# Kernel optimization log

Measured on AMD Instinct MI355X. Metric: run time of the kernel, lower is better.

Reference implementation:

```python
import jax, jax.numpy as jnp
import numpy as np


def setup_inputs() -> dict:
    key = jax.random.key(0)
    k1, k2 = jax.random.split(key)
    x = jax.random.normal(k1, (16384, 1024), dtype=jnp.float32)
    # 10 butterfly stages, each with 512 independent 2x2 mixing matrices
    Ws = jax.random.normal(k2, (10, 512, 2, 2), dtype=jnp.float32)
    return {"x": x, "Ws": Ws}


def reference(x, Ws):
    """PairLinear_MixerBlock forward for input_dim == output_dim == 2^L.
    selector and reducer are Identity; only the butterfly mixing stages remain.
    """
    bs, dim = x.shape
    n_stages = Ws.shape[0]  # log2(dim)
    y = x
    for i in range(n_stages):
        stride = 2 ** i
        # y.view(-1, 2, 2**i).permute(0, 2, 1).contiguous().view(bs, -1)
        y = y.reshape(-1, 2, stride).transpose(0, 2, 1).reshape(bs, -1)
        # PairLinear: view(bs, -1, 2) then per-pair 2x2 matmul with Ws[i]
        y = jnp.einsum('bpk,pkj->bpj', y.reshape(bs, -1, 2), Ws[i]).reshape(bs, -1)
        # y.view(-1, 2**i, 2).permute(0, 2, 1).contiguous()
        y = y.reshape(-1, stride, 2).transpose(0, 2, 1).reshape(bs, dim)
    return y
```

## Files before the change

kernel.cpp:

```cpp
#include <hip/hip_runtime.h>

#define DIM 1024
#define RPW 4
#define WAVES 4
#define ROWS_PER_BLOCK (RPW * WAVES)

__global__ __launch_bounds__(256) void butterfly_kernel(
    const float* __restrict__ x,
    const float* __restrict__ Ws,
    float* __restrict__ out,
    int rows)
{
    const int lane = threadIdx.x & 63;
    const int wave = threadIdx.x >> 6;
    const int row0 = (blockIdx.x * WAVES + wave) * RPW;

    const float4* __restrict__ Wm = (const float4*)Ws;

    float d[RPW][16];

    #pragma unroll
    for (int r = 0; r < RPW; ++r) {
        int row = row0 + r;
        if (row < rows) {
            const float4* src = (const float4*)(x + (size_t)row * DIM);
            #pragma unroll
            for (int q = 0; q < 4; ++q) {
                float4 v = src[q * 64 + lane];
                d[r][q*4+0] = v.x; d[r][q*4+1] = v.y;
                d[r][q*4+2] = v.z; d[r][q*4+3] = v.w;
            }
        } else {
            #pragma unroll
            for (int e = 0; e < 16; ++e) d[r][e] = 0.f;
        }
    }

    #pragma unroll
    for (int q = 0; q < 4; ++q) {
        int base = 0*512 + q*128 + lane*2;
        float4 m0 = Wm[base], m1 = Wm[base+1];
        #pragma unroll
        for (int r = 0; r < RPW; ++r) {
            int e = q*4;
            float u = d[r][e+0], v = d[r][e+1];
            d[r][e+0] = u*m0.x + v*m0.z;
            d[r][e+1] = u*m0.y + v*m0.w;
            u = d[r][e+2]; v = d[r][e+3];
            d[r][e+2] = u*m1.x + v*m1.z;
            d[r][e+3] = u*m1.y + v*m1.w;
        }
    }

    #pragma unroll
    for (int q = 0; q < 4; ++q) {
        int base = 1*512 + q*128 + lane*2;
        float4 m0 = Wm[base], m1 = Wm[base+1];
        #pragma unroll
        for (int r = 0; r < RPW; ++r) {
            int e = q*4;
            float u = d[r][e+0], v = d[r][e+2];
            d[r][e+0] = u*m0.x + v*m0.z;
            d[r][e+2] = u*m0.y + v*m0.w;
            u = d[r][e+1]; v = d[r][e+3];
            d[r][e+1] = u*m1.x + v*m1.z;
            d[r][e+3] = u*m1.y + v*m1.w;
        }
    }

    #pragma unroll
    for (int i = 2; i < 8; ++i) {
        const int m = 1 << (i - 2);
        const int a = (lane >> (i - 2)) & 1;
        #pragma unroll
        for (int q = 0; q < 4; ++q) {
            int P0 = (((q*64 + lane) >> (i-1)) << i) | ((lane & (m-1)) << 2);
            int base = i*512 + P0;
            float4 M0 = Wm[base+0], M1 = Wm[base+1], M2 = Wm[base+2], M3 = Wm[base+3];
            float wA0 = a ? M0.w : M0.x, wB0 = a ? M0.y : M0.z;
            float wA1 = a ? M1.w : M1.x, wB1 = a ? M1.y : M1.z;
            float wA2 = a ? M2.w : M2.x, wB2 = a ? M2.y : M2.z;
            float wA3 = a ? M3.w : M3.x, wB3 = a ? M3.y : M3.z;
            #pragma unroll
            for (int r = 0; r < RPW; ++r) {
                int e = q*4;
                float o0 = __shfl_xor(d[r][e+0], m);
                float o1 = __shfl_xor(d[r][e+1], m);
                float o2 = __shfl_xor(d[r][e+2], m);
                float o3 = __shfl_xor(d[r][e+3], m);
                d[r][e+0] = d[r][e+0]*wA0 + o0*wB0;
                d[r][e+1] = d[r][e+1]*wA1 + o1*wB1;
                d[r][e+2] = d[r][e+2]*wA2 + o2*wB2;
                d[r][e+3] = d[r][e+3]*wA3 + o3*wB3;
            }
        }
    }

    #pragma unroll
    for (int qp = 0; qp < 2; ++qp) {
        int base = 8*512 + qp*256 + lane*4;
        float4 M0 = Wm[base+0], M1 = Wm[base+1], M2 = Wm[base+2], M3 = Wm[base+3];
        #pragma unroll
        for (int r = 0; r < RPW; ++r) {
            int eu = (2*qp)*4, ev = (2*qp+1)*4;
            float u, v;
            u = d[r][eu+0]; v = d[r][ev+0]; d[r][eu+0] = u*M0.x + v*M0.z; d[r][ev+0] = u*M0.y + v*M0.w;
            u = d[r][eu+1]; v = d[r][ev+1]; d[r][eu+1] = u*M1.x + v*M1.z; d[r][ev+1] = u*M1.y + v*M1.w;
            u = d[r][eu+2]; v = d[r][ev+2]; d[r][eu+2] = u*M2.x + v*M2.z; d[r][ev+2] = u*M2.y + v*M2.w;
            u = d[r][eu+3]; v = d[r][ev+3]; d[r][eu+3] = u*M3.x + v*M3.z; d[r][ev+3] = u*M3.y + v*M3.w;
        }
    }

    #pragma unroll
    for (int qp = 0; qp < 2; ++qp) {
        int base = 9*512 + qp*256 + lane*4;
        float4 M0 = Wm[base+0], M1 = Wm[base+1], M2 = Wm[base+2], M3 = Wm[base+3];
        #pragma unroll
        for (int r = 0; r < RPW; ++r) {
            int eu = qp*4, ev = (qp+2)*4;
            float u, v;
            u = d[r][eu+0]; v = d[r][ev+0]; d[r][eu+0] = u*M0.x + v*M0.z; d[r][ev+0] = u*M0.y + v*M0.w;
            u = d[r][eu+1]; v = d[r][ev+1]; d[r][eu+1] = u*M1.x + v*M1.z; d[r][ev+1] = u*M1.y + v*M1.w;
            u = d[r][eu+2]; v = d[r][ev+2]; d[r][eu+2] = u*M2.x + v*M2.z; d[r][ev+2] = u*M2.y + v*M2.w;
            u = d[r][eu+3]; v = d[r][ev+3]; d[r][eu+3] = u*M3.x + v*M3.z; d[r][ev+3] = u*M3.y + v*M3.w;
        }
    }

    #pragma unroll
    for (int r = 0; r < RPW; ++r) {
        int row = row0 + r;
        if (row < rows) {
            float4* dst = (float4*)(out + (size_t)row * DIM);
            #pragma unroll
            for (int q = 0; q < 4; ++q) {
                float4 v;
                v.x = d[r][q*4+0]; v.y = d[r][q*4+1];
                v.z = d[r][q*4+2]; v.w = d[r][q*4+3];
                dst[q * 64 + lane] = v;
            }
        }
    }
}

extern "C" void kernel_launch(void* const* d_in, const int* in_sizes, int n_in,
                              void* d_out, int out_size, void* d_ws, size_t ws_size,
                              hipStream_t stream) {
    const float* x  = (const float*)d_in[0];
    const float* Ws = (const float*)d_in[1];
    float* out = (float*)d_out;

    int rows = in_sizes[0] / DIM;
    int grid = (rows + ROWS_PER_BLOCK - 1) / ROWS_PER_BLOCK;
    butterfly_kernel<<<grid, 256, 0, stream>>>(x, Ws, out, rows);
}
```

Before: 51.27 us.

## Pre-pack per-lane shuffle-stage weights in workspace and raise occupancy hint

```diff
diff --git a/kernel.cpp b/kernel.cpp
--- a/kernel.cpp
+++ b/kernel.cpp
@@ -4,10 +4,38 @@
 #define RPW 4
 #define WAVES 4
 #define ROWS_PER_BLOCK (RPW * WAVES)
+#define PACKED_BYTES (6 * 4 * 64 * 8 * 4)
 
-__global__ __launch_bounds__(256) void butterfly_kernel(
+
+__global__ void pack_weights(const float* __restrict__ Ws, float* __restrict__ pw) {
+    int t = blockIdx.x * blockDim.x + threadIdx.x;
+    if (t >= 6 * 4 * 64) return;
+    int lane = t & 63;
+    int q = (t >> 6) & 3;
+    int i = (t >> 8) + 2;
+    int m = 1 << (i - 2);
+    int a = (lane >> (i - 2)) & 1;
+    int P0 = (((q * 64 + lane) >> (i - 1)) << i) | ((lane & (m - 1)) << 2);
+    const float4* Wm = (const float4*)Ws;
+    float4 wa, wb;
+    float* pa = (float*)&wa;
+    float* pb = (float*)&wb;
+    #pragma unroll
+    for (int e = 0; e < 4; ++e) {
+        float4 M = Wm[i * 512 + P0 + e];
+        pa[e] = a ? M.w : M.x;
+        pb[e] = a ? M.y : M.z;
+    }
+    float4* o = (float4*)pw + (size_t)t * 2;
+    o[0] = wa;
+    o[1] = wb;
+}
+
+template <bool PACKED, int MINB>
+__global__ __launch_bounds__(256, MINB) void butterfly_kernel(
     const float* __restrict__ x,
     const float* __restrict__ Ws,
+    const float* __restrict__ pw,
     float* __restrict__ out,
     int rows)
 {
@@ -71,16 +99,25 @@
     #pragma unroll
     for (int i = 2; i < 8; ++i) {
         const int m = 1 << (i - 2);
-        const int a = (lane >> (i - 2)) & 1;
         #pragma unroll
         for (int q = 0; q < 4; ++q) {
-            int P0 = (((q*64 + lane) >> (i-1)) << i) | ((lane & (m-1)) << 2);
-            int base = i*512 + P0;
-            float4 M0 = Wm[base+0], M1 = Wm[base+1], M2 = Wm[base+2], M3 = Wm[base+3];
-            float wA0 = a ? M0.w : M0.x, wB0 = a ? M0.y : M0.z;
-            float wA1 = a ? M1.w : M1.x, wB1 = a ? M1.y : M1.z;
-            float wA2 = a ? M2.w : M2.x, wB2 = a ? M2.y : M2.z;
-            float wA3 = a ? M3.w : M3.x, wB3 = a ? M3.y : M3.z;
+            float wA0, wA1, wA2, wA3, wB0, wB1, wB2, wB3;
+            if (PACKED) {
+                const float4* wp = (const float4*)pw
+                    + ((size_t)(((i - 2) * 4 + q) * 64 + lane)) * 2;
+                float4 wa = wp[0], wb = wp[1];
+                wA0 = wa.x; wA1 = wa.y; wA2 = wa.z; wA3 = wa.w;
+                wB0 = wb.x; wB1 = wb.y; wB2 = wb.z; wB3 = wb.w;
+            } else {
+                const int a = (lane >> (i - 2)) & 1;
+                int P0 = (((q*64 + lane) >> (i-1)) << i) | ((lane & (m-1)) << 2);
+                int base = i*512 + P0;
+                float4 M0 = Wm[base+0], M1 = Wm[base+1], M2 = Wm[base+2], M3 = Wm[base+3];
+                wA0 = a ? M0.w : M0.x; wB0 = a ? M0.y : M0.z;
+                wA1 = a ? M1.w : M1.x; wB1 = a ? M1.y : M1.z;
+                wA2 = a ? M2.w : M2.x; wB2 = a ? M2.y : M2.z;
+                wA3 = a ? M3.w : M3.x; wB3 = a ? M3.y : M3.z;
+            }
             #pragma unroll
             for (int r = 0; r < RPW; ++r) {
                 int e = q*4;
@@ -151,5 +188,12 @@
 
     int rows = in_sizes[0] / DIM;
     int grid = (rows + ROWS_PER_BLOCK - 1) / ROWS_PER_BLOCK;
-    butterfly_kernel<<<grid, 256, 0, stream>>>(x, Ws, out, rows);
+
+    if (ws_size >= (size_t)PACKED_BYTES) {
+        float* pw = (float*)d_ws;
+        pack_weights<<<6, 256, 0, stream>>>(Ws, pw);
+        butterfly_kernel<true, 5><<<grid, 256, 0, stream>>>(x, Ws, pw, out, rows);
+    } else {
+        butterfly_kernel<false, 4><<<grid, 256, 0, stream>>>(x, Ws, nullptr, out, rows);
+    }
 }
```

After: 147.4 us. 188% more time.

## Compose butterfly stages into block-diagonal matrices and apply via bf16 MFMA

Applied to the files above, without the earlier changes.

```diff
diff --git a/kernel.cpp b/kernel.cpp
--- a/kernel.cpp
+++ b/kernel.cpp
@@ -1,80 +1,190 @@
 #include <hip/hip_runtime.h>
 
 #define DIM 1024
-#define RPW 4
-#define WAVES 4
-#define ROWS_PER_BLOCK (RPW * WAVES)
-
-__global__ __launch_bounds__(256) void butterfly_kernel(
+#define ROWS_PER_TILE 16
+
+typedef float  f32x4  __attribute__((ext_vector_type(4)));
+typedef short  bf16x8 __attribute__((ext_vector_type(8)));
+typedef unsigned int u32x2 __attribute__((ext_vector_type(2)));
+
+#define WF_BYTES (2 * 32 * 2 * 64 * 16)
+
+
+__device__ __forceinline__ short f2bfs(float f) {
+    union { __bf16 b; short s; } c; c.b = (__bf16)f; return c.s;
+}
+__device__ __forceinline__ unsigned f2bfbits(float f) {
+    union { __bf16 b; unsigned short u; } c; c.b = (__bf16)f; return (unsigned)c.u;
+}
+
+__global__ __launch_bounds__(64) void compose_pack(const float* __restrict__ Ws,
+                                                   short* __restrict__ wf) {
+    __shared__ float M[32 * 32];
+    const int b = blockIdx.x;
+    const int tid = threadIdx.x;
+    const bool isB = b >= 32;
+    const int grp = isB ? b - 32 : b;
+
+    for (int s = tid; s < 1024; s += 64) M[s] = ((s >> 5) == (s & 31)) ? 1.f : 0.f;
+    __syncthreads();
+
+    for (int il = 0; il < 5; ++il) {
+        #pragma unroll
+        for (int s = 0; s < 8; ++s) {
+            int task = tid + s * 64;
+            int pl = task >> 5;
+            int r  = task & 31;
+            int lo = ((pl >> il) << (il + 1)) | (pl & ((1 << il) - 1));
+            int hi = lo + (1 << il);
+            int wi = isB ? ((5 + il) * 512 + pl * 32 + grp)
+                         : (il * 512 + grp * 16 + pl);
+            const float* W = Ws + (size_t)wi * 4;
+            float w00 = W[0], w01 = W[1], w10 = W[2], w11 = W[3];
+            float u = M[r * 32 + lo], v = M[r * 32 + hi];
+            M[r * 32 + lo] = u * w00 + v * w10;
+            M[r * 32 + hi] = u * w01 + v * w11;
+        }
+        __syncthreads();
+    }
+
+    const int q = tid >> 4, lr = tid & 15;
+    #pragma unroll
+    for (int nh = 0; nh < 2; ++nh) {
+        bf16x8 fr;
+        #pragma unroll
+        for (int e = 0; e < 8; ++e)
+            fr[e] = f2bfs(M[(q * 8 + e) * 32 + nh * 16 + lr]);
+        size_t idx = (size_t)(isB ? 4096 : 0) + ((size_t)grp * 2 + nh) * 64 + tid;
+        ((bf16x8*)wf)[idx] = fr;
+    }
+}
+
+__global__ __launch_bounds__(256) void bfly_mfma(
     const float* __restrict__ x,
-    const float* __restrict__ Ws,
-    float* __restrict__ out,
-    int rows)
+    const short* __restrict__ wf1,
+    const short* __restrict__ wf2,
+    float* __restrict__ out)
+{
+    __shared__ char zt[32 * 1024];
+    const int tid = threadIdx.x;
+    const int w = tid >> 6;
+    const int l = tid & 63;
+    const int q = l >> 4, lr = l & 15;
+    const int row0 = blockIdx.x * ROWS_PER_TILE;
+
+    const f32x4 zacc = {0.f, 0.f, 0.f, 0.f};
+
+    const float* xrow = x + (size_t)(row0 + lr) * DIM;
+    #pragma unroll
+    for (int gi = 0; gi < 8; ++gi) {
+        const int g = w * 8 + gi;
+        const f32x4* xp = (const f32x4*)(xrow + g * 32 + q * 8);
+        f32x4 xa = __builtin_nontemporal_load(xp);
+        f32x4 xb = __builtin_nontemporal_load(xp + 1);
+        bf16x8 af;
+        af[0] = f2bfs(xa[0]); af[1] = f2bfs(xa[1]);
+        af[2] = f2bfs(xa[2]); af[3] = f2bfs(xa[3]);
+        af[4] = f2bfs(xb[0]); af[5] = f2bfs(xb[1]);
+        af[6] = f2bfs(xb[2]); af[7] = f2bfs(xb[3]);
+        bf16x8 b0 = ((const bf16x8*)wf1)[(g * 2 + 0) * 64 + l];
+        bf16x8 b1 = ((const bf16x8*)wf1)[(g * 2 + 1) * 64 + l];
+        f32x4 c0 = __builtin_amdgcn_mfma_f32_16x16x32_bf16(af, b0, zacc, 0, 0, 0);
+        f32x4 c1 = __builtin_amdgcn_mfma_f32_16x16x32_bf16(af, b1, zacc, 0, 0, 0);
+        #pragma unroll
+        for (int nh = 0; nh < 2; ++nh) {
+            f32x4 cc = nh ? c1 : c0;
+            int c = nh * 16 + lr;
+            unsigned lo = f2bfbits(cc[0]) | (f2bfbits(cc[1]) << 16);
+            unsigned hi = f2bfbits(cc[2]) | (f2bfbits(cc[3]) << 16);
+            int byteoff = (c * 1024 + g * 32 + q * 8) ^ ((c & 15) << 3);
+            u32x2 pk = {lo, hi};
+            *(u32x2*)(zt + byteoff) = pk;
+        }
+    }
+    __syncthreads();
+
+    f32x4 o[2][8];
+    #pragma unroll
+    for (int hh = 0; hh < 8; ++hh) {
+        const int h = w * 8 + hh;
+        bf16x8 a2;
+        #pragma unroll
+        for (int e = 0; e < 8; ++e) {
+            int byteoff = (h * 1024 + (q * 8 + e) * 32 + lr * 2) ^ ((h & 15) << 3);
+            union { unsigned short u; short s; } cv;
+            cv.u = *(const unsigned short*)(zt + byteoff);
+            a2[e] = cv.s;
+        }
+        bf16x8 b0 = ((const bf16x8*)wf2)[(h * 2 + 0) * 64 + l];
+        bf16x8 b1 = ((const bf16x8*)wf2)[(h * 2 + 1) * 64 + l];
+        o[0][hh] = __builtin_amdgcn_mfma_f32_16x16x32_bf16(a2, b0, zacc, 0, 0, 0);
+        o[1][hh] = __builtin_amdgcn_mfma_f32_16x16x32_bf16(a2, b1, zacc, 0, 0, 0);
+    }
+
+    #pragma unroll
+    for (int nh = 0; nh < 2; ++nh) {
+        #pragma unroll
+        for (int i = 0; i < 4; ++i) {
+            f32x4 v0 = { o[nh][0][i], o[nh][1][i], o[nh][2][i], o[nh][3][i] };
+            f32x4 v1 = { o[nh][4][i], o[nh][5][i], o[nh][6][i], o[nh][7][i] };
+            float* dst = out + (size_t)(row0 + q * 4 + i) * DIM
+                       + (nh * 16 + lr) * 32 + w * 8;
+            *(f32x4*)dst = v0;
+            *((f32x4*)dst + 1) = v1;
+        }
+    }
+}
+
+__global__ __launch_bounds__(256) void butterfly_fallback(
+    const float* __restrict__ x, const float* __restrict__ Ws,
+    float* __restrict__ out, int rows)
 {
     const int lane = threadIdx.x & 63;
     const int wave = threadIdx.x >> 6;
-    const int row0 = (blockIdx.x * WAVES + wave) * RPW;
-
+    const int row0 = (blockIdx.x * 4 + wave) * 2;
     const float4* __restrict__ Wm = (const float4*)Ws;
-
-    float d[RPW][16];
-
-    #pragma unroll
-    for (int r = 0; r < RPW; ++r) {
+    float d[2][16];
+    #pragma unroll
+    for (int r = 0; r < 2; ++r) {
         int row = row0 + r;
         if (row < rows) {
-            const float4* src = (const float4*)(x + (size_t)row * DIM);
+            const f32x4* src = (const f32x4*)(x + (size_t)row * DIM);
             #pragma unroll
-            for (int q = 0; q < 4; ++q) {
-                float4 v = src[q * 64 + lane];
-                d[r][q*4+0] = v.x; d[r][q*4+1] = v.y;
-                d[r][q*4+2] = v.z; d[r][q*4+3] = v.w;
+            for (int qq = 0; qq < 4; ++qq) {
+                f32x4 v = src[qq * 64 + lane];
+                d[r][qq*4+0]=v[0]; d[r][qq*4+1]=v[1]; d[r][qq*4+2]=v[2]; d[r][qq*4+3]=v[3];
             }
-        } else {
-            #pragma unroll
-            for (int e = 0; e < 16; ++e) d[r][e] = 0.f;
-        }
-    }
-
-    #pragma unroll
-    for (int q = 0; q < 4; ++q) {
-        int base = 0*512 + q*128 + lane*2;
+        } else { for (int e = 0; e < 16; ++e) d[r][e] = 0.f; }
+    }
+    #pragma unroll
+    for (int qq = 0; qq < 4; ++qq) {
+        int base = qq*128 + lane*2;
         float4 m0 = Wm[base], m1 = Wm[base+1];
         #pragma unroll
-        for (int r = 0; r < RPW; ++r) {
-            int e = q*4;
-            float u = d[r][e+0], v = d[r][e+1];
-            d[r][e+0] = u*m0.x + v*m0.z;
-            d[r][e+1] = u*m0.y + v*m0.w;
-            u = d[r][e+2]; v = d[r][e+3];
-            d[r][e+2] = u*m1.x + v*m1.z;
-            d[r][e+3] = u*m1.y + v*m1.w;
-        }
-    }
-
-    #pragma unroll
-    for (int q = 0; q < 4; ++q) {
-        int base = 1*512 + q*128 + lane*2;
+        for (int r = 0; r < 2; ++r) {
+            int e = qq*4; float u,v;
+            u=d[r][e+0]; v=d[r][e+1]; d[r][e+0]=u*m0.x+v*m0.z; d[r][e+1]=u*m0.y+v*m0.w;
+            u=d[r][e+2]; v=d[r][e+3]; d[r][e+2]=u*m1.x+v*m1.z; d[r][e+3]=u*m1.y+v*m1.w;
+        }
+    }
+    #pragma unroll
+    for (int qq = 0; qq < 4; ++qq) {
+        int base = 512 + qq*128 + lane*2;
         float4 m0 = Wm[base], m1 = Wm[base+1];
         #pragma unroll
-        for (int r = 0; r < RPW; ++r) {
-            int e = q*4;
-            float u = d[r][e+0], v = d[r][e+2];
-            d[r][e+0] = u*m0.x + v*m0.z;
-            d[r][e+2] = u*m0.y + v*m0.w;
-            u = d[r][e+1]; v = d[r][e+3];
-            d[r][e+1] = u*m1.x + v*m1.z;
-            d[r][e+3] = u*m1.y + v*m1.w;
-        }
-    }
-
+        for (int r = 0; r < 2; ++r) {
+            int e = qq*4; float u,v;
+            u=d[r][e+0]; v=d[r][e+2]; d[r][e+0]=u*m0.x+v*m0.z; d[r][e+2]=u*m0.y+v*m0.w;
+            u=d[r][e+1]; v=d[r][e+3]; d[r][e+1]=u*m1.x+v*m1.z; d[r][e+3]=u*m1.y+v*m1.w;
+        }
+    }
     #pragma unroll
     for (int i = 2; i < 8; ++i) {
         const int m = 1 << (i - 2);
-        const int a = (lane >> (i - 2)) & 1;
-        #pragma unroll
-        for (int q = 0; q < 4; ++q) {
-            int P0 = (((q*64 + lane) >> (i-1)) << i) | ((lane & (m-1)) << 2);
+        #pragma unroll
+        for (int qq = 0; qq < 4; ++qq) {
+            const int a = (lane >> (i - 2)) & 1;
+            int P0 = (((qq*64 + lane) >> (i-1)) << i) | ((lane & (m-1)) << 2);
             int base = i*512 + P0;
             float4 M0 = Wm[base+0], M1 = Wm[base+1], M2 = Wm[base+2], M3 = Wm[base+3];
             float wA0 = a ? M0.w : M0.x, wB0 = a ? M0.y : M0.z;
@@ -82,61 +192,50 @@
             float wA2 = a ? M2.w : M2.x, wB2 = a ? M2.y : M2.z;
             float wA3 = a ? M3.w : M3.x, wB3 = a ? M3.y : M3.z;
             #pragma unroll
-            for (int r = 0; r < RPW; ++r) {
-                int e = q*4;
-                float o0 = __shfl_xor(d[r][e+0], m);
-                float o1 = __shfl_xor(d[r][e+1], m);
-                float o2 = __shfl_xor(d[r][e+2], m);
-                float o3 = __shfl_xor(d[r][e+3], m);
-                d[r][e+0] = d[r][e+0]*wA0 + o0*wB0;
-                d[r][e+1] = d[r][e+1]*wA1 + o1*wB1;
-                d[r][e+2] = d[r][e+2]*wA2 + o2*wB2;
-                d[r][e+3] = d[r][e+3]*wA3 + o3*wB3;
+            for (int r = 0; r < 2; ++r) {
+                int e = qq*4;
+                float o0=__shfl_xor(d[r][e+0],m), o1=__shfl_xor(d[r][e+1],m);
+                float o2=__shfl_xor(d[r][e+2],m), o3=__shfl_xor(d[r][e+3],m);
+                d[r][e+0]=d[r][e+0]*wA0+o0*wB0; d[r][e+1]=d[r][e+1]*wA1+o1*wB1;
+                d[r][e+2]=d[r][e+2]*wA2+o2*wB2; d[r][e+3]=d[r][e+3]*wA3+o3*wB3;
             }
         }
     }
-
     #pragma unroll
     for (int qp = 0; qp < 2; ++qp) {
         int base = 8*512 + qp*256 + lane*4;
         float4 M0 = Wm[base+0], M1 = Wm[base+1], M2 = Wm[base+2], M3 = Wm[base+3];
         #pragma unroll
-        for (int r = 0; r < RPW; ++r) {
-            int eu = (2*qp)*4, ev = (2*qp+1)*4;
-            float u, v;
-            u = d[r][eu+0]; v = d[r][ev+0]; d[r][eu+0] = u*M0.x + v*M0.z; d[r][ev+0] = u*M0.y + v*M0.w;
-            u = d[r][eu+1]; v = d[r][ev+1]; d[r][eu+1] = u*M1.x + v*M1.z; d[r][ev+1] = u*M1.y + v*M1.w;
-            u = d[r][eu+2]; v = d[r][ev+2]; d[r][eu+2] = u*M2.x + v*M2.z; d[r][ev+2] = u*M2.y + v*M2.w;
-            u = d[r][eu+3]; v = d[r][ev+3]; d[r][eu+3] = u*M3.x + v*M3.z; d[r][ev+3] = u*M3.y + v*M3.w;
-        }
-    }
-
+        for (int r = 0; r < 2; ++r) {
+            int eu=(2*qp)*4, ev=(2*qp+1)*4; float u,v;
+            u=d[r][eu+0]; v=d[r][ev+0]; d[r][eu+0]=u*M0.x+v*M0.z; d[r][ev+0]=u*M0.y+v*M0.w;
+            u=d[r][eu+1]; v=d[r][ev+1]; d[r][eu+1]=u*M1.x+v*M1.z; d[r][ev+1]=u*M1.y+v*M1.w;
+            u=d[r][eu+2]; v=d[r][ev+2]; d[r][eu+2]=u*M2.x+v*M2.z; d[r][ev+2]=u*M2.y+v*M2.w;
+            u=d[r][eu+3]; v=d[r][ev+3]; d[r][eu+3]=u*M3.x+v*M3.z; d[r][ev+3]=u*M3.y+v*M3.w;
+        }
+    }
     #pragma unroll
     for (int qp = 0; qp < 2; ++qp) {
         int base = 9*512 + qp*256 + lane*4;
         float4 M0 = Wm[base+0], M1 = Wm[base+1], M2 = Wm[base+2], M3 = Wm[base+3];
         #pragma unroll
-        for (int r = 0; r < RPW; ++r) {
-            int eu = qp*4, ev = (qp+2)*4;
-            float u, v;
-            u = d[r][eu+0]; v = d[r][ev+0]; d[r][eu+0] = u*M0.x + v*M0.z; d[r][ev+0] = u*M0.y + v*M0.w;
-            u = d[r][eu+1]; v = d[r][ev+1]; d[r][eu+1] = u*M1.x + v*M1.z; d[r][ev+1] = u*M1.y + v*M1.w;
-            u = d[r][eu+2]; v = d[r][ev+2]; d[r][eu+2] = u*M2.x + v*M2.z; d[r][ev+2] = u*M2.y + v*M2.w;
-            u = d[r][eu+3]; v = d[r][ev+3]; d[r][eu+3] = u*M3.x + v*M3.z; d[r][ev+3] = u*M3.y + v*M3.w;
-        }
-    }
-
-    #pragma unroll
-    for (int r = 0; r < RPW; ++r) {
+        for (int r = 0; r < 2; ++r) {
+            int eu=qp*4, ev=(qp+2)*4; float u,v;
+            u=d[r][eu+0]; v=d[r][ev+0]; d[r][eu+0]=u*M0.x+v*M0.z; d[r][ev+0]=u*M0.y+v*M0.w;
+            u=d[r][eu+1]; v=d[r][ev+1]; d[r][eu+1]=u*M1.x+v*M1.z; d[r][ev+1]=u*M1.y+v*M1.w;
+            u=d[r][eu+2]; v=d[r][ev+2]; d[r][eu+2]=u*M2.x+v*M2.z; d[r][ev+2]=u*M2.y+v*M2.w;
+            u=d[r][eu+3]; v=d[r][ev+3]; d[r][eu+3]=u*M3.x+v*M3.z; d[r][ev+3]=u*M3.y+v*M3.w;
+        }
+    }
+    #pragma unroll
+    for (int r = 0; r < 2; ++r) {
         int row = row0 + r;
         if (row < rows) {
-            float4* dst = (float4*)(out + (size_t)row * DIM);
+            f32x4* dst = (f32x4*)(out + (size_t)row * DIM);
             #pragma unroll
-            for (int q = 0; q < 4; ++q) {
-                float4 v;
-                v.x = d[r][q*4+0]; v.y = d[r][q*4+1];
-                v.z = d[r][q*4+2]; v.w = d[r][q*4+3];
-                dst[q * 64 + lane] = v;
+            for (int qq = 0; qq < 4; ++qq) {
+                f32x4 v = { d[r][qq*4+0], d[r][qq*4+1], d[r][qq*4+2], d[r][qq*4+3] };
+                dst[qq * 64 + lane] = v;
             }
         }
     }
@@ -148,8 +247,15 @@
     const float* x  = (const float*)d_in[0];
     const float* Ws = (const float*)d_in[1];
     float* out = (float*)d_out;
-
     int rows = in_sizes[0] / DIM;
-    int grid = (rows + ROWS_PER_BLOCK - 1) / ROWS_PER_BLOCK;
-    butterfly_kernel<<<grid, 256, 0, stream>>>(x, Ws, out, rows);
-}
+
+    if (ws_size >= (size_t)WF_BYTES && (rows % ROWS_PER_TILE) == 0) {
+        short* wf1 = (short*)d_ws;
+        short* wf2 = (short*)d_ws + 32768;
+        compose_pack<<<64, 64, 0, stream>>>(Ws, (short*)d_ws);
+        bfly_mfma<<<rows / ROWS_PER_TILE, 256, 0, stream>>>(x, wf1, wf2, out);
+    } else {
+        int grid = (rows + 7) / 8;
+        butterfly_fallback<<<grid, 256, 0, stream>>>(x, Ws, out, rows);
+    }
+}
```

After: 60.53 us. +18.1%, slower.
